# Performance work log

Hardware: AMD Instinct MI355X
Metric: run time of the kernel (lower is better)

Reference implementation:

```python
import jax, jax.numpy as jnp
import numpy as np
import math


def pos_enc_3d(h, w, d, c):
    # Faithful PositionalEncoding3D: channels = ceil(c/6)*2 (made even), sin/cos per axis.
    cpe = int(np.ceil(c / 6) * 2)
    if cpe % 2:
        cpe += 1
    inv_freq = 1.0 / (10000.0 ** (np.arange(0, cpe, 2, dtype=np.float32) / cpe))

    def axis_emb(n):
        s = np.arange(n, dtype=np.float32)[:, None] * inv_freq  # (n, cpe//2)
        return np.concatenate([np.sin(s), np.cos(s)], axis=-1)  # (n, cpe)

    ex = np.broadcast_to(axis_emb(h)[:, None, None, :], (h, w, d, cpe))
    ey = np.broadcast_to(axis_emb(w)[None, :, None, :], (h, w, d, cpe))
    ez = np.broadcast_to(axis_emb(d)[None, None, :, :], (h, w, d, cpe))
    emb = np.concatenate([ex, ey, ez], axis=-1)[..., :c]  # (h,w,d,c)
    return jnp.asarray(np.transpose(emb, (3, 0, 1, 2)))  # (c,h,w,d)


def conv3d(x, w, b):
    # x: (b,c,h,w,d), w: (o,i,3,3,3), padding=1
    y = jax.lax.conv_general_dilated(
        x, w, window_strides=(1, 1, 1), padding=[(1, 1)] * 3,
        dimension_numbers=('NCHWD', 'OIHWD', 'NCHWD'))
    return y + b[None, :, None, None, None]


def setup_inputs() -> dict:
    key = jax.random.key(0)
    ks = jax.random.split(key, 12)
    B, C, H, W, D = 2, 64, 16, 16, 16
    C8 = C // 8
    s_emb = 1.0 / math.sqrt(C)
    s_conv = 1.0 / math.sqrt(C * 27)
    return {
        'x': jax.random.normal(ks[0], (B, C, H, W, D), dtype=jnp.float32),
        'Wq': jax.random.normal(ks[1], (C, C), dtype=jnp.float32) * s_emb,
        'Wk': jax.random.normal(ks[2], (C, C), dtype=jnp.float32) * s_emb,
        'Wv': jax.random.normal(ks[3], (C, C), dtype=jnp.float32) * s_emb,
        'qw': jax.random.normal(ks[4], (C8, C, 3, 3, 3), dtype=jnp.float32) * s_conv,
        'qb': jax.random.normal(ks[5], (C8,), dtype=jnp.float32) * 0.01,
        'kw': jax.random.normal(ks[6], (C8, C, 3, 3, 3), dtype=jnp.float32) * s_conv,
        'kb': jax.random.normal(ks[7], (C8,), dtype=jnp.float32) * 0.01,
        'vw': jax.random.normal(ks[8], (C, C, 3, 3, 3), dtype=jnp.float32) * s_conv,
        'vb': jax.random.normal(ks[9], (C,), dtype=jnp.float32) * 0.01,
        'lam1': jax.random.normal(ks[10], (1,), dtype=jnp.float32) * 0.5,
        'lam2': jax.random.normal(ks[11], (1,), dtype=jnp.float32) * 0.5,
    }


def reference(x, Wq, Wk, Wv, qw, qb, kw, kb, vw, vb, lam1, lam2):
    b, c, h, w, d = x.shape
    n = h * w * d
    # NOTE: torch code does `x += pe` in-place inside SelfAttention, so the
    # PE-added x is also what GSA and the residual see.
    pe = pos_enc_3d(h, w, d, c)  # (c,h,w,d)
    x_pe = x + pe[None]

    # ---- SelfAttention (TSA) ----
    tok = x_pe.reshape(b, c, n).transpose(0, 2, 1)  # (b,n,c)
    Q = jnp.einsum('bnc,cd->bnd', tok, Wq)
    K = jnp.einsum('bnc,cd->bnd', tok, Wk)
    V = jnp.einsum('bnc,cd->bnd', tok, Wv)
    A = jax.nn.softmax(jnp.einsum('bic,bjc->bij', Q, K) / math.sqrt(c), axis=-1)
    tsa = jnp.einsum('bij,bjc->bic', A, V).transpose(0, 2, 1).reshape(b, c, h, w, d)

    # ---- GlobalSpatialAttention (GSA) ----
    M = conv3d(x_pe, qw, qb).reshape(b, c // 8, n)   # (b,c/8,n)
    Nk = conv3d(x_pe, kw, kb).reshape(b, c // 8, n)  # (b,c/8,n)
    Wv_ = conv3d(x_pe, vw, vb).reshape(b, c, n)      # (b,c,n)
    Bm = jax.nn.softmax(jnp.einsum('bci,bcj->bij', M, Nk), axis=-1)  # (b,n,n)
    gsa = jnp.einsum('bcj,bij->bci', Wv_, Bm).reshape(b, c, h, w, d)

    return lam1[0] * tsa + lam2[0] * gsa + x_pe
```

## Files before the change

kernel.cpp:

```cpp
#include <hip/hip_runtime.h>
#include <math.h>

#define BB 2
#define CC 64
#define NN 4096
#define CN (CC*NN)
#define NJ 8
#define NT ((NN/NJ)/64)

#define LOG2E 1.4426950408889634f
#define QSCALE 0.18033688011112042f

#define XT_ROWS 4097
#define WQKV_OFF (27*80*64)

typedef __attribute__((ext_vector_type(8))) short short8;
typedef __attribute__((ext_vector_type(4))) float float4v;
typedef unsigned short ushortT;

__device__ __forceinline__ ushortT f2bf(float x) {
    union { float f; unsigned u; } v; v.f = x;
    unsigned r = v.u + 0x7FFF + ((v.u >> 16) & 1);
    return (ushortT)(r >> 16);
}
__device__ __forceinline__ float bf2f(short s) {
    union { unsigned u; float f; } v;
    v.u = ((unsigned)(unsigned short)s) << 16;
    return v.f;
}
__device__ __forceinline__ unsigned pk2(float a, float b) {
    unsigned ua = __float_as_uint(a) + 0x8000u;
    unsigned ub = __float_as_uint(b) + 0x8000u;
    return __builtin_amdgcn_perm(ub, ua, 0x07060302);
}

__device__ __forceinline__ float pe_tab_val(int c, int pos) {
    int c2 = (c < 22) ? c : (c < 44) ? (c - 22) : (c - 44);
    int is_cos = (c2 >= 11);
    int k = c2 - (is_cos ? 11 : 0);
    float freq = exp2f(-1.2079738526863135f * (float)k);
    float arg = (float)pos * freq;
    return is_cos ? cosf(arg) : sinf(arg);
}

__global__ __launch_bounds__(256) void k_pre(const float* __restrict__ x,
                                             const float* __restrict__ qw,
                                             const float* __restrict__ kw,
                                             const float* __restrict__ vw,
                                             const float* __restrict__ Wq,
                                             const float* __restrict__ Wk,
                                             const float* __restrict__ Wv,
                                             float* __restrict__ xpe,
                                             ushortT* __restrict__ Xt,
                                             ushortT* __restrict__ Wr) {
    int blk = blockIdx.x, t = threadIdx.x;
    if (blk < 256) {
        __shared__ float sPE[64][17];
        __shared__ float sT[64][33];
        int b = blk >> 7, pos0 = (blk & 127) * 32;
        #pragma unroll
        for (int k = 0; k < 4; k++) {
            int e = t + k * 256;
            int c = e >> 4, coord = e & 15;
            sPE[c][coord] = pe_tab_val(c, coord);
        }
        __syncthreads();
        int pin = t & 31, cg = t >> 5;
        #pragma unroll
        for (int pass = 0; pass < 8; pass++) {
            int c = pass * 8 + cg;
            int pos = pos0 + pin;
            int coord = (c < 22) ? (pos >> 8) : (c < 44) ? ((pos >> 4) & 15) : (pos & 15);
            size_t gi = (size_t)(b * 64 + c) * NN + pos;
            float v = x[gi] + sPE[c][coord];
            xpe[gi] = v;
            sT[c][pin] = v;
        }
        __syncthreads();
        int icn = t & 63, pg = t >> 6;
        #pragma unroll
        for (int pass = 0; pass < 8; pass++) {
            int po = pass * 4 + pg;
            Xt[((size_t)b * XT_ROWS + pos0 + po + 1) * 64 + icn] = f2bf(sT[icn][po]);
        }
        if ((blk & 127) == 0 && t < 64)
            Xt[((size_t)b * XT_ROWS) * 64 + t] = 0;
    } else {
        int idx = (blk - 256) * 256 + t;
        if (idx < WQKV_OFF) {
            int ic = idx & 63;
            int oc = (idx >> 6) % 80;
            int tap = idx / 5120;
            float v;
            if (oc < 8)       v = qw[(oc * 64 + ic) * 27 + tap] * LOG2E;
            else if (oc < 16) v = kw[((oc - 8) * 64 + ic) * 27 + tap];
            else              v = vw[((oc - 16) * 64 + ic) * 27 + tap];
            Wr[idx] = f2bf(v);
        } else if (idx < WQKV_OFF + 3 * 64 * 64) {
            int idx2 = idx - WQKV_OFF;
            int c = idx2 & 63, d = (idx2 >> 6) & 63, mat = idx2 >> 12;
            const float* Wm = (mat == 0) ? Wq : (mat == 1) ? Wk : Wv;
            float v = Wm[c * 64 + d] * ((mat == 0) ? QSCALE : 1.f);
            Wr[idx] = f2bf(v);
        }
    }
}

__global__ __launch_bounds__(256) void k_qkv(const ushortT* __restrict__ Xt,
                                             const ushortT* __restrict__ Wr,
                                             ushortT* __restrict__ Qb,
                                             ushortT* __restrict__ Kb,
                                             ushortT* __restrict__ Vtb) {
    __shared__ ushortT sVt[64][72];
    int t = threadIdx.x, w = t >> 6, l = t & 63;
    int lane15 = l & 15, q = l >> 4;
    int mat = blockIdx.y, b = blockIdx.z;
    int i0 = blockIdx.x * 64 + w * 16;

    const ushortT* Wt = Wr + WQKV_OFF + mat * 4096;
    const ushortT* xrow = Xt + ((size_t)b * XT_ROWS + i0 + lane15 + 1) * 64;
    short8 a0 = *(const short8*)(xrow + q * 8);
    short8 a1 = *(const short8*)(xrow + 32 + q * 8);
    float4v acc[4];
    #pragma unroll
    for (int cg = 0; cg < 4; cg++) {
        const ushortT* wrow = Wt + (cg * 16 + lane15) * 64;
        short8 b0 = *(const short8*)(wrow + q * 8);
        short8 b1 = *(const short8*)(wrow + 32 + q * 8);
        float4v a = (float4v)0.f;
        a = __builtin_amdgcn_mfma_f32_16x16x32_bf16(a0, b0, a, 0, 0, 0);
        a = __builtin_amdgcn_mfma_f32_16x16x32_bf16(a1, b1, a, 0, 0, 0);
        acc[cg] = a;
    }
    if (mat < 2) {
        ushortT* o = (mat == 0) ? Qb : Kb;
        #pragma unroll
        for (int cg = 0; cg < 4; cg++)
            #pragma unroll
            for (int r = 0; r < 4; r++)
                o[((size_t)(b * NN + i0 + q * 4 + r)) * 64 + cg * 16 + lane15] = f2bf(acc[cg][r]);
    } else {
        int il = w * 16 + q * 4;
        #pragma unroll
        for (int cg = 0; cg < 4; cg++)
            #pragma unroll
            for (int r = 0; r < 4; r++)
                sVt[cg * 16 + lane15][il + r] = f2bf(acc[cg][r]);
        __syncthreads();
        int c2 = t >> 2, seg = t & 3;
        short8 v0 = *(const short8*)&sVt[c2][seg * 16];
        short8 v1 = *(const short8*)&sVt[c2][seg * 16 + 8];
        size_t base = ((size_t)(b * 64 + c2)) * NN + blockIdx.x * 64 + seg * 16;
        *(short8*)(Vtb + base) = v0;
        *(short8*)(Vtb + base + 8) = v1;
    }
}

template<int IS_TSA>
__device__ __forceinline__ void stage_load(short8* kst, short8* vst,
                                           const ushortT* __restrict__ Km,
                                           const ushortT* __restrict__ Vt,
                                           int b, int jb, int t) {
    if (IS_TSA) {
        #pragma unroll
        for (int ps = 0; ps < 2; ps++) {
            int idx = ps * 256 + t, j = idx >> 3, g = idx & 7;
            kst[ps] = *(const short8*)(Km + ((size_t)(b * NN + jb + j)) * 64 + g * 8);
        }
    } else {
        if (t < 64)
            kst[0] = *(const short8*)(Km + ((size_t)(b * NN + jb + t)) * 8);
    }
    #pragma unroll
    for (int ps = 0; ps < 2; ps++) {
        int idx = ps * 256 + t, c = idx >> 3, gj = idx & 7;
        vst[ps] = *(const short8*)(Vt + ((size_t)(b * 64 + c)) * NN + jb + gj * 8);
    }
}

template<int IS_TSA>
__device__ __forceinline__ void stage_write(const short8* kst, const short8* vst,
                                            ushortT* sK, ushortT* sV, int t) {
    if (IS_TSA) {
        #pragma unroll
        for (int ps = 0; ps < 2; ps++) {
            int idx = ps * 256 + t, j = idx >> 3, g = idx & 7;
            *(short8*)(sK + j * 64 + ((g ^ (j & 7)) * 8)) = kst[ps];
        }
    } else {
        if (t < 64)
            *(short8*)(sK + t * 64 + ((t & 7) * 8)) = kst[0];
    }
    #pragma unroll
    for (int ps = 0; ps < 2; ps++) {
        int idx = ps * 256 + t, c = idx >> 3, gj = idx & 7;
        *(short8*)(sV + c * 64 + ((gj ^ (c & 7)) * 8)) = vst[ps];
    }
}

template<int IS_TSA>
__device__ __forceinline__ void flash_body(int it, int jc, int b, int t,
                                           const ushortT* __restrict__ Qm,
                                           const ushortT* __restrict__ Km,
                                           const ushortT* __restrict__ Vt,
                                           float* __restrict__ pM,
                                           float* __restrict__ pL,
                                           ushortT* __restrict__ pAcc,
                                           ushortT* __restrict__ sKb,
                                           ushortT* __restrict__ sVb,
                                           ushortT* __restrict__ sPall) {
    constexpr int KCH = IS_TSA ? 2 : 1;
    constexpr int DQ  = IS_TSA ? 64 : 8;
    int w = t >> 6, l = t & 63;
    int lane15 = l & 15, q = l >> 4;
    int i0a = it * 128 + w * 16;
    ushortT* myP = sPall + w * (16 * 64);

    short8 qf[2][KCH];
    #pragma unroll
    for (int si = 0; si < 2; si++) {
        const ushortT* qrow = Qm + ((size_t)(b * NN + i0a + si * 64 + lane15)) * DQ;
        if (IS_TSA) {
            qf[si][0] = *(const short8*)(qrow + q * 8);
            qf[si][1] = *(const short8*)(qrow + 32 + q * 8);
        } else {
            short8 z = (short8)0;
            if (q == 0) z = *(const short8*)qrow;
            qf[si][0] = z;
        }
    }

    float m_run[2] = {-3e38f, -3e38f}, Lacc[2] = {0.f, 0.f};
    float4v O[2][4];
    #pragma unroll
    for (int si = 0; si < 2; si++)
        #pragma unroll
        for (int cs = 0; cs < 4; cs++) O[si][cs] = (float4v)0.f;

    const int jbase0 = jc * (NN / NJ);

    short8 kst[2], vst[2];
    stage_load<IS_TSA>(kst, vst, Km, Vt, b, jbase0, t);
    stage_write<IS_TSA>(kst, vst, sKb, sVb, t);
    __syncthreads();

    for (int jt = 0; jt < NT; jt++) {
        int cur = jt & 1;
        ushortT* cK = sKb + cur * 4096;
        ushortT* cV = sVb + cur * 4096;
        bool more = (jt + 1 < NT);

        if (more) stage_load<IS_TSA>(kst, vst, Km, Vt, b, jbase0 + (jt + 1) * 64, t);

        short8 kf[4][KCH];
        #pragma unroll
        for (int sub = 0; sub < 4; sub++) {
            int jr = sub * 16 + lane15;
            if (IS_TSA) {
                kf[sub][0] = *(const short8*)(cK + jr * 64 + (((0 * 4 + q) ^ (lane15 & 7)) * 8));
                kf[sub][1] = *(const short8*)(cK + jr * 64 + (((1 * 4 + q) ^ (lane15 & 7)) * 8));
            } else {
                short8 z = (short8)0;
                if (q == 0) z = *(const short8*)(cK + jr * 64 + ((lane15 & 7) * 8));
                kf[sub][0] = z;
            }
        }

        float4v s[2][4];
        #pragma unroll
        for (int si = 0; si < 2; si++)
            #pragma unroll
            for (int sub = 0; sub < 4; sub++) {
                float4v acc = (float4v)0.f;
                #pragma unroll
                for (int kc = 0; kc < KCH; kc++)
                    acc = __builtin_amdgcn_mfma_f32_16x16x32_bf16(kf[sub][kc], qf[si][kc], acc, 0, 0, 0);
                s[si][sub] = acc;
            }

        short8 va[4], vbf[4];
        #pragma unroll
        for (int sub = 0; sub < 4; sub++) {
            int cr = sub * 16 + lane15;
            va[sub]  = *(const short8*)(cV + cr * 64 + ((q ^ (lane15 & 7)) * 8));
            vbf[sub] = *(const short8*)(cV + cr * 64 + (((4 + q) ^ (lane15 & 7)) * 8));
        }

        #pragma unroll
        for (int si = 0; si < 2; si++) {
            float tmax = fmaxf(fmaxf(fmaxf(s[si][0][0], s[si][0][1]), fmaxf(s[si][0][2], s[si][0][3])),
                               fmaxf(fmaxf(s[si][1][0], s[si][1][1]), fmaxf(s[si][1][2], s[si][1][3])));
            float tmax2 = fmaxf(fmaxf(fmaxf(s[si][2][0], s[si][2][1]), fmaxf(s[si][2][2], s[si][2][3])),
                                fmaxf(fmaxf(s[si][3][0], s[si][3][1]), fmaxf(s[si][3][2], s[si][3][3])));
            tmax = fmaxf(tmax, tmax2);
            tmax = fmaxf(tmax, __shfl_xor(tmax, 16));
            tmax = fmaxf(tmax, __shfl_xor(tmax, 32));
            float mnew = fmaxf(m_run[si], tmax);

            if (__any(mnew > m_run[si])) {
                float corr = exp2f(m_run[si] - mnew);
                Lacc[si] *= corr;
                float c0 = __shfl(corr, q * 4 + 0);
                float c1 = __shfl(corr, q * 4 + 1);
                float c2 = __shfl(corr, q * 4 + 2);
                float c3 = __shfl(corr, q * 4 + 3);
                #pragma unroll
                for (int cs = 0; cs < 4; cs++) {
                    O[si][cs][0] *= c0; O[si][cs][1] *= c1;
                    O[si][cs][2] *= c2; O[si][cs][3] *= c3;
                }
            }
            m_run[si] = mnew;

            #pragma unroll
            for (int sub = 0; sub < 4; sub++) {
                float p0 = exp2f(s[si][sub][0] - mnew);
                float p1 = exp2f(s[si][sub][1] - mnew);
                float p2 = exp2f(s[si][sub][2] - mnew);
                float p3 = exp2f(s[si][sub][3] - mnew);
                Lacc[si] += (p0 + p1) + (p2 + p3);
                unsigned lo = pk2(p0, p1), hi = pk2(p2, p3);
                int g = sub * 2 + (q >> 1);
                unsigned* wp = (unsigned*)(myP + lane15 * 64 + ((g ^ (lane15 & 7)) * 8) + (q & 1) * 4);
                wp[0] = lo; wp[1] = hi;
            }

            short8 pf0 = *(const short8*)(myP + lane15 * 64 + (((0 * 4 + q) ^ (lane15 & 7)) * 8));
            short8 pf1 = *(const short8*)(myP + lane15 * 64 + (((1 * 4 + q) ^ (lane15 & 7)) * 8));

            #pragma unroll
            for (int sub = 0; sub < 4; sub++) {
                O[si][sub] = __builtin_amdgcn_mfma_f32_16x16x32_bf16(pf0, va[sub], O[si][sub], 0, 0, 0);
                O[si][sub] = __builtin_amdgcn_mfma_f32_16x16x32_bf16(pf1, vbf[sub], O[si][sub], 0, 0, 0);
            }
        }

        if (more)
            stage_write<IS_TSA>(kst, vst, sKb + (cur ^ 1) * 4096, sVb + (cur ^ 1) * 4096, t);
        __syncthreads();
    }

    #pragma unroll
    for (int si = 0; si < 2; si++) {
        size_t base = (size_t)(b * NJ + jc) * NN + i0a + si * 64;
        float Ls = Lacc[si];
        Ls += __shfl_xor(Ls, 16);
        Ls += __shfl_xor(Ls, 32);
        if (q == 0) {
            pL[base + lane15] = Ls;
            pM[base + lane15] = m_run[si];
        }
        #pragma unroll
        for (int cs = 0; cs < 4; cs++)
            #pragma unroll
            for (int r = 0; r < 4; r++)
                pAcc[(base + q * 4 + r) * 64 + cs * 16 + lane15] = f2bf(O[si][cs][r]);
    }
}

__global__ __launch_bounds__(256, 3) void k_tsacv(const ushortT* __restrict__ Qb,
                                                  const ushortT* __restrict__ Kb,
                                                  const ushortT* __restrict__ Vtb,
                                                  const ushortT* __restrict__ Xt,
                                                  const ushortT* __restrict__ Wr,
                                                  const float* __restrict__ qb,
                                                  const float* __restrict__ kb,
                                                  const float* __restrict__ vb,
                                                  ushortT* __restrict__ Mt,
                                                  ushortT* __restrict__ Nt,
                                                  ushortT* __restrict__ Wvt,
                                                  float* __restrict__ pMt, float* __restrict__ pLt,
                                                  ushortT* __restrict__ pAccT) {
    __shared__ ushortT sm[20480];
    int bx = blockIdx.x, t = threadIdx.x;
    if (bx >= 128) {
        int fb = bx - 128;
        int it = fb & 31, jc = (fb >> 5) & 7, b = fb >> 8;
        flash_body<1>(it, jc, b, t, Qb, Kb, Vtb, pMt, pLt, pAccT,
                      sm, sm + 8192, sm + 16384);
    } else {
        int cv = bx;
        int tile = cv & 63, b = cv >> 6;
        int w = t >> 6, l = t & 63, lane15 = l & 15, q = l >> 4;
        int pos0 = tile * 64 + w * 16;
        const ushortT* xb = Xt + (size_t)b * XT_ROWS * 64;
        int pos = pos0 + lane15;
        int dz = pos & 15, wy = (pos >> 4) & 15, hx = pos >> 8;

        ushortT* sW = sm;

        float4v accA[5], accB[5];
        #pragma unroll
        for (int o = 0; o < 5; o++) { accA[o] = (float4v)0.f; accB[o] = (float4v)0.f; }

        short8 ws[3];
        auto ldW = [&](int tap) {
            #pragma unroll
            for (int c3 = 0; c3 < 3; c3++) {
                int idx = t + c3 * 256;
                if (idx < 640)
                    ws[c3] = *(const short8*)(Wr + (size_t)tap * 5120 + idx * 8);
            }
        };
        auto wrW = [&](ushortT* buf) {
            #pragma unroll
            for (int c3 = 0; c3 < 3; c3++) {
                int idx = t + c3 * 256;
                if (idx < 640) {
                    int row = idx >> 3, g = idx & 7;
                    *(short8*)(buf + row * 64 + ((g ^ (row & 7)) * 8)) = ws[c3];
                }
            }
        };

        ldW(0);
        wrW(sW);
        __syncthreads();

        #pragma unroll
        for (int tap = 0; tap < 27; tap++) {
            const int dh = tap / 9 - 1, dw = (tap / 3) % 3 - 1, dd = tap % 3 - 1;
            const int shift = dh * 256 + dw * 16 + dd;
            ushortT* cW = sW + (tap & 1) * 5120;
            bool more = (tap + 1 < 27);

            if (more) ldW(tap + 1);

            bool ok = ((unsigned)(hx + dh) < 16u) &&
                      ((unsigned)(wy + dw) < 16u) &&
                      ((unsigned)(dz + dd) < 16u);
            int row = ok ? (pos + shift + 1) : 0;
            const ushortT* xrow = xb + (size_t)row * 64 + q * 8;
            short8 b0 = *(const short8*)xrow;
            short8 b1 = *(const short8*)(xrow + 32);

            #pragma unroll
            for (int o = 0; o < 5; o++) {
                int wr2 = o * 16 + lane15;
                short8 a0 = *(const short8*)(cW + wr2 * 64 + ((q ^ (lane15 & 7)) * 8));
                short8 a1 = *(const short8*)(cW + wr2 * 64 + (((4 + q) ^ (lane15 & 7)) * 8));
                accA[o] = __builtin_amdgcn_mfma_f32_16x16x32_bf16(a0, b0, accA[o], 0, 0, 0);
                accB[o] = __builtin_amdgcn_mfma_f32_16x16x32_bf16(a1, b1, accB[o], 0, 0, 0);
            }

            if (more) wrW(sW + ((tap + 1) & 1) * 5120);
            __syncthreads();
        }

        #pragma unroll
        for (int o = 0; o < 5; o++) {
            float4v accT = accA[o] + accB[o];
            if (o == 0) {
                #pragma unroll
                for (int r = 0; r < 4; r++) {
                    int ol = q * 4 + r;
                    float v = accT[r];
                    if (ol < 8)
                        Mt[((size_t)(b * NN + pos)) * 8 + ol] = f2bf(v + qb[ol] * LOG2E);
                    else
                        Nt[((size_t)(b * NN + pos)) * 8 + (ol - 8)] = f2bf(v + kb[ol - 8]);
                }
            } else {
                #pragma unroll
                for (int r = 0; r < 4; r++) {
                    int oc = (o - 1) * 16 + q * 4 + r;
                    Wvt[((size_t)(b * 64 + oc)) * NN + pos] = f2bf(accT[r] + vb[oc]);
                }
            }
        }
    }
}

__global__ __launch_bounds__(256, 3) void k_gsa(const ushortT* __restrict__ Mtb,
                                                const ushortT* __restrict__ Ntb,
                                                const ushortT* __restrict__ Wvtb,
                                                float* __restrict__ pMg, float* __restrict__ pLg,
                                                ushortT* __restrict__ pAccG) {
    __shared__ ushortT sK[2][64 * 64];
    __shared__ ushortT sV[2][64 * 64];
    __shared__ ushortT sP[4][16 * 64];
    int t = threadIdx.x;
    flash_body<0>(blockIdx.x, blockIdx.y, blockIdx.z, t, Mtb, Ntb, Wvtb, pMg, pLg, pAccG,
                  &sK[0][0], &sV[0][0], &sP[0][0]);
}

__device__ __forceinline__ void reduce_set(const float* __restrict__ pM,
                                           const float* __restrict__ pL,
                                           const ushortT* __restrict__ pAcc,
                                           int b, int n, int seg, float* v) {
    float mv[NJ], M = -3e38f;
    #pragma unroll
    for (int jcc = 0; jcc < NJ; jcc++) {
        mv[jcc] = pM[(size_t)(b * NJ + jcc) * NN + n];
        M = fmaxf(M, mv[jcc]);
    }
    float L = 0.f;
    #pragma unroll
    for (int e = 0; e < 8; e++) v[e] = 0.f;
    #pragma unroll
    for (int jcc = 0; jcc < NJ; jcc++) {
        size_t rb = (size_t)(b * NJ + jcc) * NN + n;
        float wgt = exp2f(mv[jcc] - M);
        L += pL[rb] * wgt;
        short8 x0 = *(const short8*)(pAcc + rb * 64 + seg * 8);
        #pragma unroll
        for (int e = 0; e < 8; e++) v[e] += wgt * bf2f(x0[e]);
    }
    float invL = 1.f / L;
    #pragma unroll
    for (int e = 0; e < 8; e++) v[e] *= invL;
}

__global__ __launch_bounds__(256) void k_reduce(const float* __restrict__ pMt,
                                                const float* __restrict__ pLt,
                                                const ushortT* __restrict__ pAccT,
                                                const float* __restrict__ pMg,
                                                const float* __restrict__ pLg,
                                                const ushortT* __restrict__ pAccG,
                                                const float* __restrict__ xpe,
                                                const float* __restrict__ lam1,
                                                const float* __restrict__ lam2,
                                                float* __restrict__ out) {
    __shared__ float sT[32][65];
    __shared__ float sG[32][65];
    int t = threadIdx.x;
    int b = blockIdx.y;
    int n0 = blockIdx.x * 32;
    int pp = t >> 3, seg = t & 7;
    int n = n0 + pp;

    float vt[8], vg[8];
    reduce_set(pMt, pLt, pAccT, b, n, seg, vt);
    reduce_set(pMg, pLg, pAccG, b, n, seg, vg);
    #pragma unroll
    for (int e = 0; e < 8; e++) {
        sT[pp][seg * 8 + e] = vt[e];
        sG[pp][seg * 8 + e] = vg[e];
    }
    __syncthreads();

    int c = t >> 2, ns = (t & 3) * 8;
    float la1 = lam1[0], la2 = lam2[0];
    size_t ob = ((size_t)(b * 64 + c)) * NN + n0 + ns;
    const float* xp = xpe + ob;
    #pragma unroll
    for (int j = 0; j < 8; j += 4) {
        float4 ov;
        ov.x = la1 * sT[ns + j + 0][c] + la2 * sG[ns + j + 0][c] + xp[j + 0];
        ov.y = la1 * sT[ns + j + 1][c] + la2 * sG[ns + j + 1][c] + xp[j + 1];
        ov.z = la1 * sT[ns + j + 2][c] + la2 * sG[ns + j + 2][c] + xp[j + 2];
        ov.w = la1 * sT[ns + j + 3][c] + la2 * sG[ns + j + 3][c] + xp[j + 3];
        *(float4*)(out + ob + j) = ov;
    }
}

extern "C" void kernel_launch(void* const* d_in, const int* in_sizes, int n_in,
                              void* d_out, int out_size, void* d_ws, size_t ws_size,
                              hipStream_t stream) {
    const float* x    = (const float*)d_in[0];
    const float* Wq   = (const float*)d_in[1];
    const float* Wk   = (const float*)d_in[2];
    const float* Wv   = (const float*)d_in[3];
    const float* qw   = (const float*)d_in[4];
    const float* qb   = (const float*)d_in[5];
    const float* kw   = (const float*)d_in[6];
    const float* kb   = (const float*)d_in[7];
    const float* vw   = (const float*)d_in[8];
    const float* vb   = (const float*)d_in[9];
    const float* lam1 = (const float*)d_in[10];
    const float* lam2 = (const float*)d_in[11];
    float* out = (float*)d_out;

    char* W = (char*)d_ws;
    float*   xpe   = (float*)(W);
    ushortT* Qb    = (ushortT*)(W + (2u << 20));
    ushortT* Kb    = (ushortT*)(W + (3u << 20));
    ushortT* Vtb   = (ushortT*)(W + (4u << 20));
    ushortT* Mtb   = (ushortT*)(W + (5u << 20));
    ushortT* Ntb   = (ushortT*)(W + (5u << 20) + (1u << 17));
    ushortT* Wvtb  = (ushortT*)(W + (5u << 20) + (2u << 17));
    ushortT* Xt    = (ushortT*)(W + (6u << 20) + (2u << 17));
    ushortT* Wr    = (ushortT*)(W + (7u << 20) + (1u << 19));
    float*   pLt   = (float*)(W + (8u << 20));
    float*   pLg   = (float*)(W + (8u << 20) + (1u << 18));
    float*   pMt   = (float*)(W + (8u << 20) + (2u << 18));
    float*   pMg   = (float*)(W + (8u << 20) + (3u << 18));
    ushortT* pAccT = (ushortT*)(W + (9u << 20));
    ushortT* pAccG = (ushortT*)(W + (17u << 20));

    k_pre<<<dim3(256 + (WQKV_OFF + 3 * 64 * 64 + 255) / 256), dim3(256), 0, stream>>>(
        x, qw, kw, vw, Wq, Wk, Wv, xpe, Xt, Wr);
    k_qkv<<<dim3(64, 3, BB), dim3(256), 0, stream>>>(Xt, Wr, Qb, Kb, Vtb);
    k_tsacv<<<dim3(128 + 32 * NJ * BB), dim3(256), 0, stream>>>(
        Qb, Kb, Vtb, Xt, Wr, qb, kb, vb, Mtb, Ntb, Wvtb, pMt, pLt, pAccT);
    k_gsa<<<dim3(32, NJ, BB), dim3(256), 0, stream>>>(
        Mtb, Ntb, Wvtb, pMg, pLg, pAccG);
    k_reduce<<<dim3(NN / 32, BB), dim3(256), 0, stream>>>(
        pMt, pLt, pAccT, pMg, pLg, pAccG, xpe, lam1, lam2, out);
}
```

Measured before the change: 135.3 us.

## Fuse QKV projection into preprocessing and overlap TSA reduction with GSA

Folds the separate QKV projection kernel into k_pre. Each block now handles 64 positions and computes Q, K and V^T by MFMA directly from the PE-added tile in shared memory, with weights converted on the fly. The TSA partial reduction (writing lam1*tsa + x_pe to out) is moved into extra blocks of the GSA flash kernel so it runs concurrently. A separate small kernel then adds lam2*gsa in place. This removes one launch and the intermediate weight staging, and overlaps the reduction with GSA compute, at the cost of an extra read-modify-write of the output and fewer preprocessing blocks.

```diff
diff --git a/kernel.cpp b/kernel.cpp
--- a/kernel.cpp
+++ b/kernel.cpp
@@ -52,12 +52,18 @@
                                              const float* __restrict__ Wv,
                                              float* __restrict__ xpe,
                                              ushortT* __restrict__ Xt,
-                                             ushortT* __restrict__ Wr) {
+                                             ushortT* __restrict__ Wr,
+                                             ushortT* __restrict__ Qb,
+                                             ushortT* __restrict__ Kb,
+                                             ushortT* __restrict__ Vtb) {
     int blk = blockIdx.x, t = threadIdx.x;
-    if (blk < 256) {
+    if (blk < 128) {
+        __shared__ float sT[64][65];
         __shared__ float sPE[64][17];
-        __shared__ float sT[64][33];
-        int b = blk >> 7, pos0 = (blk & 127) * 32;
+        __shared__ ushortT sWt[64][72];
+        __shared__ ushortT sVt[64][72];
+        int b = blk >> 6, pos0 = (blk & 63) * 64;
+
         #pragma unroll
         for (int k = 0; k < 4; k++) {
             int e = t + k * 256;
@@ -65,10 +71,11 @@
             sPE[c][coord] = pe_tab_val(c, coord);
         }
         __syncthreads();
-        int pin = t & 31, cg = t >> 5;
-        #pragma unroll
-        for (int pass = 0; pass < 8; pass++) {
-            int c = pass * 8 + cg;
+
+        int pin = t & 63, cg0 = t >> 6;
+        #pragma unroll
+        for (int pass = 0; pass < 16; pass++) {
+            int c = pass * 4 + cg0;
             int pos = pos0 + pin;
             int coord = (c < 22) ? (pos >> 8) : (c < 44) ? ((pos >> 4) & 15) : (pos & 15);
             size_t gi = (size_t)(b * 64 + c) * NN + pos;
@@ -77,16 +84,83 @@
             sT[c][pin] = v;
         }
         __syncthreads();
-        int icn = t & 63, pg = t >> 6;
-        #pragma unroll
-        for (int pass = 0; pass < 8; pass++) {
-            int po = pass * 4 + pg;
-            Xt[((size_t)b * XT_ROWS + pos0 + po + 1) * 64 + icn] = f2bf(sT[icn][po]);
-        }
-        if ((blk & 127) == 0 && t < 64)
-            Xt[((size_t)b * XT_ROWS) * 64 + t] = 0;
+
+        {
+            int icn = t & 63, pg = t >> 6;
+            #pragma unroll
+            for (int pass = 0; pass < 16; pass++) {
+                int po = pass * 4 + pg;
+                Xt[((size_t)b * XT_ROWS + pos0 + po + 1) * 64 + icn] = f2bf(sT[icn][po]);
+            }
+            if ((blk & 63) == 0 && t < 64)
+                Xt[((size_t)b * XT_ROWS) * 64 + t] = 0;
+        }
+
+        int w = t >> 6, l = t & 63, lane15 = l & 15, q = l >> 4;
+        int row = w * 16 + lane15;
+        short8 a0, a1;
+        {
+            union { ushortT u[8]; short8 s; } t0, t1;
+            #pragma unroll
+            for (int e = 0; e < 8; e++) {
+                t0.u[e] = f2bf(sT[q * 8 + e][row]);
+                t1.u[e] = f2bf(sT[32 + q * 8 + e][row]);
+            }
+            a0 = t0.s; a1 = t1.s;
+        }
+
+        #pragma unroll
+        for (int mat = 0; mat < 3; mat++) {
+            const float* Wm = (mat == 0) ? Wq : (mat == 1) ? Wk : Wv;
+            float sc = (mat == 0) ? QSCALE : 1.f;
+            __syncthreads();
+            #pragma unroll
+            for (int p = 0; p < 4; p++) {
+                int idx = t + p * 256;
+                int c = idx >> 4, d4 = (idx & 15) * 4;
+                float4 wv = *(const float4*)&Wm[c * 64 + d4];
+                sWt[d4 + 0][c] = f2bf(wv.x * sc);
+                sWt[d4 + 1][c] = f2bf(wv.y * sc);
+                sWt[d4 + 2][c] = f2bf(wv.z * sc);
+                sWt[d4 + 3][c] = f2bf(wv.w * sc);
+            }
+            __syncthreads();
+
+            float4v acc[4];
+            #pragma unroll
+            for (int cg = 0; cg < 4; cg++) {
+                const ushortT* wrow = &sWt[cg * 16 + lane15][0];
+                short8 b0 = *(const short8*)(wrow + q * 8);
+                short8 b1 = *(const short8*)(wrow + 32 + q * 8);
+                float4v a = (float4v)0.f;
+                a = __builtin_amdgcn_mfma_f32_16x16x32_bf16(a0, b0, a, 0, 0, 0);
+                a = __builtin_amdgcn_mfma_f32_16x16x32_bf16(a1, b1, a, 0, 0, 0);
+                acc[cg] = a;
+            }
+            if (mat < 2) {
+                ushortT* o = (mat == 0) ? Qb : Kb;
+                #pragma unroll
+                for (int cg = 0; cg < 4; cg++)
+                    #pragma unroll
+                    for (int r = 0; r < 4; r++)
+                        o[((size_t)(b * NN + pos0 + w * 16 + q * 4 + r)) * 64 + cg * 16 + lane15] = f2bf(acc[cg][r]);
+            } else {
+                #pragma unroll
+                for (int cg = 0; cg < 4; cg++)
+                    #pragma unroll
+                    for (int r = 0; r < 4; r++)
+                        sVt[cg * 16 + lane15][w * 16 + q * 4 + r] = f2bf(acc[cg][r]);
+                __syncthreads();
+                int c2 = t >> 2, seg = t & 3;
+                short8 v0 = *(const short8*)&sVt[c2][seg * 16];
+                short8 v1 = *(const short8*)&sVt[c2][seg * 16 + 8];
+                size_t base = ((size_t)(b * 64 + c2)) * NN + pos0 + seg * 16;
+                *(short8*)(Vtb + base) = v0;
+                *(short8*)(Vtb + base + 8) = v1;
+            }
+        }
     } else {
-        int idx = (blk - 256) * 256 + t;
+        int idx = (blk - 128) * 256 + t;
         if (idx < WQKV_OFF) {
             int ic = idx & 63;
             int oc = (idx >> 6) % 80;
@@ -96,63 +170,7 @@
             else if (oc < 16) v = kw[((oc - 8) * 64 + ic) * 27 + tap];
             else              v = vw[((oc - 16) * 64 + ic) * 27 + tap];
             Wr[idx] = f2bf(v);
-        } else if (idx < WQKV_OFF + 3 * 64 * 64) {
-            int idx2 = idx - WQKV_OFF;
-            int c = idx2 & 63, d = (idx2 >> 6) & 63, mat = idx2 >> 12;
-            const float* Wm = (mat == 0) ? Wq : (mat == 1) ? Wk : Wv;
-            float v = Wm[c * 64 + d] * ((mat == 0) ? QSCALE : 1.f);
-            Wr[idx] = f2bf(v);
-        }
-    }
-}
-
-__global__ __launch_bounds__(256) void k_qkv(const ushortT* __restrict__ Xt,
-                                             const ushortT* __restrict__ Wr,
-                                             ushortT* __restrict__ Qb,
-                                             ushortT* __restrict__ Kb,
-                                             ushortT* __restrict__ Vtb) {
-    __shared__ ushortT sVt[64][72];
-    int t = threadIdx.x, w = t >> 6, l = t & 63;
-    int lane15 = l & 15, q = l >> 4;
-    int mat = blockIdx.y, b = blockIdx.z;
-    int i0 = blockIdx.x * 64 + w * 16;
-
-    const ushortT* Wt = Wr + WQKV_OFF + mat * 4096;
-    const ushortT* xrow = Xt + ((size_t)b * XT_ROWS + i0 + lane15 + 1) * 64;
-    short8 a0 = *(const short8*)(xrow + q * 8);
-    short8 a1 = *(const short8*)(xrow + 32 + q * 8);
-    float4v acc[4];
-    #pragma unroll
-    for (int cg = 0; cg < 4; cg++) {
-        const ushortT* wrow = Wt + (cg * 16 + lane15) * 64;
-        short8 b0 = *(const short8*)(wrow + q * 8);
-        short8 b1 = *(const short8*)(wrow + 32 + q * 8);
-        float4v a = (float4v)0.f;
-        a = __builtin_amdgcn_mfma_f32_16x16x32_bf16(a0, b0, a, 0, 0, 0);
-        a = __builtin_amdgcn_mfma_f32_16x16x32_bf16(a1, b1, a, 0, 0, 0);
-        acc[cg] = a;
-    }
-    if (mat < 2) {
-        ushortT* o = (mat == 0) ? Qb : Kb;
-        #pragma unroll
-        for (int cg = 0; cg < 4; cg++)
-            #pragma unroll
-            for (int r = 0; r < 4; r++)
-                o[((size_t)(b * NN + i0 + q * 4 + r)) * 64 + cg * 16 + lane15] = f2bf(acc[cg][r]);
-    } else {
-        int il = w * 16 + q * 4;
-        #pragma unroll
-        for (int cg = 0; cg < 4; cg++)
-            #pragma unroll
-            for (int r = 0; r < 4; r++)
-                sVt[cg * 16 + lane15][il + r] = f2bf(acc[cg][r]);
-        __syncthreads();
-        int c2 = t >> 2, seg = t & 3;
-        short8 v0 = *(const short8*)&sVt[c2][seg * 16];
-        short8 v1 = *(const short8*)&sVt[c2][seg * 16 + 8];
-        size_t base = ((size_t)(b * 64 + c2)) * NN + blockIdx.x * 64 + seg * 16;
-        *(short8*)(Vtb + base) = v0;
-        *(short8*)(Vtb + base + 8) = v1;
+        }
     }
 }
 
@@ -356,6 +374,33 @@
             for (int r = 0; r < 4; r++)
                 pAcc[(base + q * 4 + r) * 64 + cs * 16 + lane15] = f2bf(O[si][cs][r]);
     }
+}
+
+__device__ __forceinline__ void reduce_set(const float* __restrict__ pM,
+                                           const float* __restrict__ pL,
+                                           const ushortT* __restrict__ pAcc,
+                                           int b, int n, int seg, float* v) {
+    float mv[NJ], M = -3e38f;
+    #pragma unroll
+    for (int jcc = 0; jcc < NJ; jcc++) {
+        mv[jcc] = pM[(size_t)(b * NJ + jcc) * NN + n];
+        M = fmaxf(M, mv[jcc]);
+    }
+    float L = 0.f;
+    #pragma unroll
+    for (int e = 0; e < 8; e++) v[e] = 0.f;
+    #pragma unroll
+    for (int jcc = 0; jcc < NJ; jcc++) {
+        size_t rb = (size_t)(b * NJ + jcc) * NN + n;
+        float wgt = exp2f(mv[jcc] - M);
+        L += pL[rb] * wgt;
+        short8 x0 = *(const short8*)(pAcc + rb * 64 + seg * 8);
+        #pragma unroll
+        for (int e = 0; e < 8; e++) v[e] += wgt * bf2f(x0[e]);
+    }
+    float invL = 1.f / L;
+    #pragma unroll
+    for (int e = 0; e < 8; e++) v[e] *= invL;
 }
 
 __global__ __launch_bounds__(256, 3) void k_tsacv(const ushortT* __restrict__ Qb,
@@ -475,53 +520,52 @@
                                                 const ushortT* __restrict__ Ntb,
                                                 const ushortT* __restrict__ Wvtb,
                                                 float* __restrict__ pMg, float* __restrict__ pLg,
-                                                ushortT* __restrict__ pAccG) {
-    __shared__ ushortT sK[2][64 * 64];
-    __shared__ ushortT sV[2][64 * 64];
-    __shared__ ushortT sP[4][16 * 64];
-    int t = threadIdx.x;
-    flash_body<0>(blockIdx.x, blockIdx.y, blockIdx.z, t, Mtb, Ntb, Wvtb, pMg, pLg, pAccG,
-                  &sK[0][0], &sV[0][0], &sP[0][0]);
-}
-
-__device__ __forceinline__ void reduce_set(const float* __restrict__ pM,
-                                           const float* __restrict__ pL,
-                                           const ushortT* __restrict__ pAcc,
-                                           int b, int n, int seg, float* v) {
-    float mv[NJ], M = -3e38f;
-    #pragma unroll
-    for (int jcc = 0; jcc < NJ; jcc++) {
-        mv[jcc] = pM[(size_t)(b * NJ + jcc) * NN + n];
-        M = fmaxf(M, mv[jcc]);
-    }
-    float L = 0.f;
-    #pragma unroll
-    for (int e = 0; e < 8; e++) v[e] = 0.f;
-    #pragma unroll
-    for (int jcc = 0; jcc < NJ; jcc++) {
-        size_t rb = (size_t)(b * NJ + jcc) * NN + n;
-        float wgt = exp2f(mv[jcc] - M);
-        L += pL[rb] * wgt;
-        short8 x0 = *(const short8*)(pAcc + rb * 64 + seg * 8);
-        #pragma unroll
-        for (int e = 0; e < 8; e++) v[e] += wgt * bf2f(x0[e]);
-    }
-    float invL = 1.f / L;
-    #pragma unroll
-    for (int e = 0; e < 8; e++) v[e] *= invL;
-}
-
-__global__ __launch_bounds__(256) void k_reduce(const float* __restrict__ pMt,
+                                                ushortT* __restrict__ pAccG,
+                                                const float* __restrict__ pMt,
                                                 const float* __restrict__ pLt,
                                                 const ushortT* __restrict__ pAccT,
-                                                const float* __restrict__ pMg,
-                                                const float* __restrict__ pLg,
-                                                const ushortT* __restrict__ pAccG,
                                                 const float* __restrict__ xpe,
                                                 const float* __restrict__ lam1,
-                                                const float* __restrict__ lam2,
                                                 float* __restrict__ out) {
-    __shared__ float sT[32][65];
+    __shared__ ushortT sm[20480];
+    int bx = blockIdx.x, t = threadIdx.x;
+    if (bx < 512) {
+        int it = bx & 31, jc = (bx >> 5) & 7, b = bx >> 8;
+        flash_body<0>(it, jc, b, t, Mtb, Ntb, Wvtb, pMg, pLg, pAccG,
+                      sm, sm + 8192, sm + 16384);
+    } else {
+        int rb = bx - 512;
+        int b = rb >> 7, n0 = (rb & 127) * 32;
+        float (*sT_)[65] = (float(*)[65])sm;
+        int pp = t >> 3, seg = t & 7, n = n0 + pp;
+
+        float vt[8];
+        reduce_set(pMt, pLt, pAccT, b, n, seg, vt);
+        #pragma unroll
+        for (int e = 0; e < 8; e++) sT_[pp][seg * 8 + e] = vt[e];
+        __syncthreads();
+
+        int c = t >> 2, ns = (t & 3) * 8;
+        float la1 = lam1[0];
+        size_t ob = ((size_t)(b * 64 + c)) * NN + n0 + ns;
+        const float* xp = xpe + ob;
+        #pragma unroll
+        for (int j = 0; j < 8; j += 4) {
+            float4 ov;
+            ov.x = la1 * sT_[ns + j + 0][c] + xp[j + 0];
+            ov.y = la1 * sT_[ns + j + 1][c] + xp[j + 1];
+            ov.z = la1 * sT_[ns + j + 2][c] + xp[j + 2];
+            ov.w = la1 * sT_[ns + j + 3][c] + xp[j + 3];
+            *(float4*)(out + ob + j) = ov;
+        }
+    }
+}
+
+__global__ __launch_bounds__(256) void k_reduce_g(const float* __restrict__ pMg,
+                                                  const float* __restrict__ pLg,
+                                                  const ushortT* __restrict__ pAccG,
+                                                  const float* __restrict__ lam2,
+                                                  float* __restrict__ out) {
     __shared__ float sG[32][65];
     int t = threadIdx.x;
     int b = blockIdx.y;
@@ -529,28 +573,23 @@
     int pp = t >> 3, seg = t & 7;
     int n = n0 + pp;
 
-    float vt[8], vg[8];
-    reduce_set(pMt, pLt, pAccT, b, n, seg, vt);
+    float vg[8];
     reduce_set(pMg, pLg, pAccG, b, n, seg, vg);
     #pragma unroll
-    for (int e = 0; e < 8; e++) {
-        sT[pp][seg * 8 + e] = vt[e];
-        sG[pp][seg * 8 + e] = vg[e];
-    }
+    for (int e = 0; e < 8; e++) sG[pp][seg * 8 + e] = vg[e];
     __syncthreads();
 
     int c = t >> 2, ns = (t & 3) * 8;
-    float la1 = lam1[0], la2 = lam2[0];
+    float la2 = lam2[0];
     size_t ob = ((size_t)(b * 64 + c)) * NN + n0 + ns;
-    const float* xp = xpe + ob;
     #pragma unroll
     for (int j = 0; j < 8; j += 4) {
-        float4 ov;
-        ov.x = la1 * sT[ns + j + 0][c] + la2 * sG[ns + j + 0][c] + xp[j + 0];
-        ov.y = la1 * sT[ns + j + 1][c] + la2 * sG[ns + j + 1][c] + xp[j + 1];
-        ov.z = la1 * sT[ns + j + 2][c] + la2 * sG[ns + j + 2][c] + xp[j + 2];
-        ov.w = la1 * sT[ns + j + 3][c] + la2 * sG[ns + j + 3][c] + xp[j + 3];
-        *(float4*)(out + ob + j) = ov;
+        float4 cur = *(const float4*)(out + ob + j);
+        cur.x += la2 * sG[ns + j + 0][c];
+        cur.y += la2 * sG[ns + j + 1][c];
+        cur.z += la2 * sG[ns + j + 2][c];
+        cur.w += la2 * sG[ns + j + 3][c];
+        *(float4*)(out + ob + j) = cur;
     }
 }
 
@@ -588,13 +627,12 @@
     ushortT* pAccT = (ushortT*)(W + (9u << 20));
     ushortT* pAccG = (ushortT*)(W + (17u << 20));
 
-    k_pre<<<dim3(256 + (WQKV_OFF + 3 * 64 * 64 + 255) / 256), dim3(256), 0, stream>>>(
-        x, qw, kw, vw, Wq, Wk, Wv, xpe, Xt, Wr);
-    k_qkv<<<dim3(64, 3, BB), dim3(256), 0, stream>>>(Xt, Wr, Qb, Kb, Vtb);
+    k_pre<<<dim3(128 + WQKV_OFF / 256), dim3(256), 0, stream>>>(
+        x, qw, kw, vw, Wq, Wk, Wv, xpe, Xt, Wr, Qb, Kb, Vtb);
     k_tsacv<<<dim3(128 + 32 * NJ * BB), dim3(256), 0, stream>>>(
         Qb, Kb, Vtb, Xt, Wr, qb, kb, vb, Mtb, Ntb, Wvtb, pMt, pLt, pAccT);
-    k_gsa<<<dim3(32, NJ, BB), dim3(256), 0, stream>>>(
-        Mtb, Ntb, Wvtb, pMg, pLg, pAccG);
-    k_reduce<<<dim3(NN / 32, BB), dim3(256), 0, stream>>>(
-        pMt, pLt, pAccT, pMg, pLg, pAccG, xpe, lam1, lam2, out);
-}
+    k_gsa<<<dim3(512 + 256), dim3(256), 0, stream>>>(
+        Mtb, Ntb, Wvtb, pMg, pLg, pAccG, pMt, pLt, pAccT, xpe, lam1, out);
+    k_reduce_g<<<dim3(NN / 32, BB), dim3(256), 0, stream>>>(
+        pMg, pLg, pAccG, lam2, out);
+}
```

Measured after the change: 135.0 us. About the same (-0.2%).
